# Performance work log

Measured on AMD Instinct MI355X. Metric: run time of the kernel, lower is better.

Reference implementation:

```python
import jax, jax.numpy as jnp
import numpy as np

LN_EPS = 1e-5

def _layernorm(x, w, b):
    mu = jnp.mean(x, axis=-1, keepdims=True)
    var = jnp.mean((x - mu) ** 2, axis=-1, keepdims=True)
    return (x - mu) * jax.lax.rsqrt(var + LN_EPS) * w + b

def _parallel_scan(A, B, x):
    # A, B, x: (Bb, L, S). Log-space cumsum trick, faithful to torch version.
    A_safe = jnp.clip(A, 0.001, 0.999)
    log_A = jnp.log(A_safe + 1e-10)
    log_cum_A = jnp.cumsum(log_A, axis=1)
    log_cum_A_max = jnp.max(log_cum_A, axis=1, keepdims=True)
    log_cum_A_c = log_cum_A - log_cum_A_max
    cum_A = jnp.exp(log_cum_A_c)
    BX = B * x
    # shifted (exclusive) centered log-cumsum: zeros at t=0
    zeros = jnp.zeros_like(log_cum_A_c[:, :1])
    log_cum_shift = jnp.concatenate([zeros, log_cum_A_c[:, :-1]], axis=1)
    BX_norm = BX * jnp.exp(-log_cum_shift)
    cum_BX = jnp.cumsum(BX_norm, axis=1)
    return cum_BX * cum_A

def setup_inputs() -> dict:
    key = jax.random.key(0)
    ks = jax.random.split(key, 8)
    Bb, L, D, S = 16, 4096, 512, 64
    def xavier(k, shape, gain):
        fan_out, fan_in = shape
        std = gain * np.sqrt(2.0 / (fan_in + fan_out))
        return jax.random.normal(k, shape, jnp.float32) * std
    x = jax.random.normal(ks[0], (Bb, L, D), jnp.float32)
    Wx = xavier(ks[1], (S, D), 0.5)
    Wdt = xavier(ks[2], (S, D), 1.0)
    WB = xavier(ks[3], (S, D), 0.4)
    WC = xavier(ks[4], (S, D), 0.4)
    Wout = xavier(ks[5], (D, S), 0.5)
    # A_init = -rand*0.8 - 0.2 ; A_log = log(-A_init) = log(uniform(0.2, 1.0))
    A_log = jnp.log(jax.random.uniform(ks[6], (S,), jnp.float32, 0.2, 1.0))
    return {
        "x": x,
        "ln_w": jnp.ones((D,), jnp.float32),
        "ln_b": jnp.zeros((D,), jnp.float32),
        "Wx": Wx, "bx": jnp.zeros((S,), jnp.float32),
        "Wdt": Wdt, "bdt": jnp.zeros((S,), jnp.float32),
        "A_log": A_log,
        "WB": WB, "WC": WC,
        "Dp": jnp.zeros((D,), jnp.float32),
        "Wout": Wout, "bout": jnp.zeros((D,), jnp.float32),
    }

def reference(x, ln_w, ln_b, Wx, bx, Wdt, bdt, A_log, WB, WC, Dp, Wout, bout):
    x_norm = _layernorm(x, ln_w, ln_b)                       # (B,L,D)
    delta = jax.nn.softplus(x_norm @ Wdt.T + bdt) * 0.01 + 0.0001  # (B,L,S)
    B_t = x_norm @ WB.T                                      # (B,L,S)
    C_t = x_norm @ WC.T                                      # (B,L,S)
    A = -jnp.exp(A_log)                                      # (S,)
    x_proj = x_norm @ Wx.T + bx                              # (B,L,S)
    deltaA = jnp.clip(delta * A, -10.0, -0.0001)
    A_disc = jnp.exp(deltaA)
    B_disc = delta * B_t
    h = _parallel_scan(A_disc, B_disc, x_proj)               # (B,L,S)
    y = C_t * h
    y = jnp.where(jnp.any(~jnp.isfinite(y)), jnp.zeros_like(y), y)
    y = y @ Wout.T + bout                                    # (B,L,D)
    D_safe = jnp.clip(Dp, -2.0, 2.0)
    return y + D_safe * x
```

## Files before the change

kernel.cpp:

```cpp
#include <hip/hip_runtime.h>
#include <hip/hip_bf16.h>
#include <math.h>

typedef __attribute__((ext_vector_type(4))) float  floatx4;
typedef __attribute__((ext_vector_type(8))) short  shortx8;
typedef unsigned short ushort_t;
typedef unsigned int   uint32;

#define BB 16
#define LL 4096
#define DD 512
#define SS 64
#define NTOK (BB*LL)
#define NCH 64

__device__ __forceinline__ ushort_t f2bf(float f) {
    uint32 u = __float_as_uint(f);
    u += 0x7FFFu + ((u >> 16) & 1u);
    return (ushort_t)(u >> 16);
}
__device__ __forceinline__ float bf2f(ushort_t u) {
    return __uint_as_float(((uint32)u) << 16);
}
__device__ __forceinline__ uint32 pack2(float lo, float hi) {
    __hip_bfloat162 h = __float22bfloat162_rn(make_float2(lo, hi));
    union { __hip_bfloat162 h; uint32 u; } cv; cv.h = h;
    return cv.u;
}

__device__ __forceinline__ void gload16(const void* g, void* l) {
    __builtin_amdgcn_global_load_lds(
        (const __attribute__((address_space(1))) unsigned int*)g,
        (__attribute__((address_space(3))) unsigned int*)l, 16, 0, 0);
}

__global__ __launch_bounds__(256) void k_prep(
    const float* __restrict__ Wdt, const float* __restrict__ WB,
    const float* __restrict__ WC,  const float* __restrict__ Wx,
    const float* __restrict__ Wout,
    const float* __restrict__ lnw, const float* __restrict__ lnb,
    ushort_t* __restrict__ wcat, ushort_t* __restrict__ woutb,
    float* __restrict__ u, float* __restrict__ c)
{
    const int bid = blockIdx.x;
    if (bid < 64) {
        const int wave = threadIdx.x >> 6, lane = threadIdx.x & 63;
        const int n = bid * 4 + wave;
        const float* src = (n < 64) ? Wdt : (n < 128) ? WB : (n < 192) ? WC : Wx;
        const float* row = src + (size_t)(n & 63) * 512;
        float4 a  = *(const float4*)(row + lane * 8);
        float4 b  = *(const float4*)(row + lane * 8 + 4);
        float4 wa = *(const float4*)(lnw + lane * 8);
        float4 wb = *(const float4*)(lnw + lane * 8 + 4);
        float4 ba = *(const float4*)(lnb + lane * 8);
        float4 bb = *(const float4*)(lnb + lane * 8 + 4);
        float w0 = a.x * wa.x, w1 = a.y * wa.y, w2 = a.z * wa.z, w3 = a.w * wa.w;
        float w4 = b.x * wb.x, w5 = b.y * wb.y, w6 = b.z * wb.z, w7 = b.w * wb.w;
        float us = w0 + w1 + w2 + w3 + w4 + w5 + w6 + w7;
        float cs = a.x*ba.x + a.y*ba.y + a.z*ba.z + a.w*ba.w
                 + b.x*bb.x + b.y*bb.y + b.z*bb.z + b.w*bb.w;
        uint4 o;
        o.x = (uint32)f2bf(w0) | ((uint32)f2bf(w1) << 16);
        o.y = (uint32)f2bf(w2) | ((uint32)f2bf(w3) << 16);
        o.z = (uint32)f2bf(w4) | ((uint32)f2bf(w5) << 16);
        o.w = (uint32)f2bf(w6) | ((uint32)f2bf(w7) << 16);
        ((uint4*)(wcat + (size_t)n * 512))[lane] = o;
        #pragma unroll
        for (int off = 32; off > 0; off >>= 1) {
            us += __shfl_xor(us, off);
            cs += __shfl_xor(cs, off);
        }
        if (lane == 0) { u[n] = us; c[n] = cs; }
    } else {
        int idx = (bid - 64) * 2048 + threadIdx.x * 8;
        float4 a = *(const float4*)(Wout + idx);
        float4 b = *(const float4*)(Wout + idx + 4);
        uint4 o;
        o.x = (uint32)f2bf(a.x) | ((uint32)f2bf(a.y) << 16);
        o.y = (uint32)f2bf(a.z) | ((uint32)f2bf(a.w) << 16);
        o.z = (uint32)f2bf(b.x) | ((uint32)f2bf(b.y) << 16);
        o.w = (uint32)f2bf(b.z) | ((uint32)f2bf(b.w) << 16);
        *(uint4*)(woutb + idx) = o;
    }
}

__global__ __launch_bounds__(512, 4) void k_proj(
    const float* __restrict__ x, const ushort_t* __restrict__ wcat,
    const float* __restrict__ u, const float* __restrict__ c,
    const float* __restrict__ bdt, const float* __restrict__ bx_, const float* __restrict__ A_log,
    float* __restrict__ Ap, float* __restrict__ BXv, ushort_t* __restrict__ Ctb,
    float* __restrict__ Asum, float* __restrict__ Bsum)
{
    __shared__ __align__(16) char sBuf[49152];
    __shared__ float sMu[128], sRs[128];
    ushort_t* sA = (ushort_t*)sBuf;
    ushort_t* sB = (ushort_t*)(sBuf + 16384);
    float*    sPA = (float*)sBuf;
    float*    sPB = sPA + 2 * 64 * 17;

    const int tid  = threadIdx.x;
    const int wave = tid >> 6, lane = tid & 63;
    const int ln   = lane & 15, qd = lane >> 4;
    const int mh   = wave >> 2, nq = wave & 3;
    const int token0 = blockIdx.x * 128;

    int tB[4], cB[4];
    #pragma unroll
    for (int r = 0; r < 4; r++) { int sl = r * 512 + tid; tB[r] = sl >> 3; cB[r] = ((sl & 7) ^ (tB[r] & 7)) * 8; }
    int rowA[2], k8A[2];
    #pragma unroll
    for (int r = 0; r < 2; r++) { int sl = r * 512 + tid; rowA[r] = sl >> 3; k8A[r] = sl & 7; }

    floatx4 acc[4][4] = {};
    float sacc[2] = {0.f, 0.f}, qacc[2] = {0.f, 0.f};

    for (int kc = 0; kc < 8; kc++) {
        const int kb = kc * 64;
        #pragma unroll
        for (int r = 0; r < 4; r++)
            gload16(wcat + (size_t)tB[r] * DD + kb + cB[r],
                    sBuf + 16384 + r * 8192 + wave * 1024);
        #pragma unroll
        for (int r = 0; r < 2; r++) {
            const float4* xp = (const float4*)(x + (size_t)(token0 + rowA[r]) * DD + kb + k8A[r] * 8);
            float4 v0 = xp[0], v1 = xp[1];
            sacc[r] += (v0.x + v0.y) + (v0.z + v0.w) + (v1.x + v1.y) + (v1.z + v1.w);
            qacc[r] += v0.x*v0.x + v0.y*v0.y + v0.z*v0.z + v0.w*v0.w
                     + v1.x*v1.x + v1.y*v1.y + v1.z*v1.z + v1.w*v1.w;
            uint4 pk;
            pk.x = pack2(v0.x, v0.y);
            pk.y = pack2(v0.z, v0.w);
            pk.z = pack2(v1.x, v1.y);
            pk.w = pack2(v1.z, v1.w);
            *(uint4*)(sBuf + rowA[r] * 128 + ((k8A[r] ^ (rowA[r] & 7)) << 4)) = pk;
        }
        __syncthreads();
        #pragma unroll
        for (int ks8 = 0; ks8 < 8; ks8 += 4) {
            shortx8 af[4], bf[4];
            #pragma unroll
            for (int mt = 0; mt < 4; mt++) {
                int t = mh * 64 + mt * 16 + ln;
                af[mt] = *(const shortx8*)&sA[t * 64 + (((ks8 + qd) ^ (ln & 7)) << 3)];
            }
            #pragma unroll
            for (int nt = 0; nt < 4; nt++) {
                int n = nt * 64 + nq * 16 + ln;
                bf[nt] = *(const shortx8*)&sB[n * 64 + (((ks8 + qd) ^ (ln & 7)) << 3)];
            }
            #pragma unroll
            for (int mt = 0; mt < 4; mt++)
                #pragma unroll
                for (int nt = 0; nt < 4; nt++)
                    acc[mt][nt] = __builtin_amdgcn_mfma_f32_16x16x32_bf16(
                        af[mt], bf[nt], acc[mt][nt], 0, 0, 0);
        }
        __syncthreads();
    }

    #pragma unroll
    for (int r = 0; r < 2; r++) {
        float s_ = sacc[r], q_ = qacc[r];
        s_ += __shfl_xor(s_, 1); q_ += __shfl_xor(q_, 1);
        s_ += __shfl_xor(s_, 2); q_ += __shfl_xor(q_, 2);
        s_ += __shfl_xor(s_, 4); q_ += __shfl_xor(q_, 4);
        if ((lane & 7) == 0) {
            int row = r * 64 + wave * 8 + (lane >> 3);
            float mu = s_ * (1.0f / 512.0f);
            sMu[row] = mu;
            sRs[row] = rsqrtf(q_ * (1.0f / 512.0f) - mu * mu + 1e-5f);
        }
    }
    __syncthreads();

    {
        const int s = nq * 16 + ln;
        float bdt_s = bdt[s], bx_s = bx_[s];
        float A_s = -expf(A_log[s]);
        float u0 = u[s], u1 = u[64 + s], u2 = u[128 + s], u3 = u[192 + s];
        float c0 = c[s], c1 = c[64 + s], c2 = c[128 + s], c3 = c[192 + s];
        const bool fc = ((blockIdx.x & 31) == 0) && (mh == 0);
        #pragma unroll
        for (int mt = 0; mt < 4; mt++) {
            float Al = 1.f, Bl = 0.f;
            #pragma unroll
            for (int r = 0; r < 4; r++) {
                int tl  = mt * 16 + qd * 4 + r;
                int tok = token0 + mh * 64 + tl;
                float mu_t = sMu[mh * 64 + tl], rs_t = sRs[mh * 64 + tl];
                float zdt = rs_t * (acc[mt][0][r] - mu_t * u0) + c0;
                float zb  = rs_t * (acc[mt][1][r] - mu_t * u1) + c1;
                float zc  = rs_t * (acc[mt][2][r] - mu_t * u2) + c2;
                float zx  = rs_t * (acc[mt][3][r] - mu_t * u3) + c3;
                float zin = zdt + bdt_s;
                float sp  = fmaxf(zin, 0.0f) + log1pf(expf(-fabsf(zin)));
                float delta = sp * 0.01f + 1e-4f;
                float dA    = fminf(fmaxf(delta * A_s, -10.0f), -1e-4f);
                float a     = fminf(fmaxf(expf(dA), 0.001f), 0.999f) + 1e-10f;
                float bxv   = delta * zb * (zx + bx_s);
                size_t g = (size_t)tok * 64 + s;
                Ap[g] = a; BXv[g] = bxv; Ctb[g] = f2bf(zc);
                bool first = fc && (tl == 0);
                float alpha = first ? 0.f : a;
                float beta  = first ? bxv : a * bxv;
                Al *= alpha;
                Bl = fmaf(alpha, Bl, beta);
            }
            sPA[(mh * 64 + s) * 17 + mt * 4 + qd] = Al;
            sPB[(mh * 64 + s) * 17 + mt * 4 + qd] = Bl;
        }
    }
    __syncthreads();
    if (tid < 128) {
        int ch = tid >> 6, ss = tid & 63;
        const float* pa = &sPA[(ch * 64 + ss) * 17];
        const float* pb = &sPB[(ch * 64 + ss) * 17];
        float A = pa[0], B = pb[0];
        #pragma unroll
        for (int g = 1; g < 16; g++) {
            A *= pa[g];
            B = fmaf(pa[g], B, pb[g]);
        }
        int o = (blockIdx.x * 2 + ch) * 64 + ss;
        Asum[o] = A; Bsum[o] = B;
    }
}

__global__ __launch_bounds__(256) void k_scan(
    const float* __restrict__ Ap, const float* __restrict__ BXv, const ushort_t* __restrict__ Ctb,
    const float* __restrict__ Asum, const float* __restrict__ Bsum,
    ushort_t* __restrict__ P)
{
    __shared__ float sAs[4096], sBs[4096];
    const int tid = threadIdx.x;
    const int b = blockIdx.x >> 4, cq = blockIdx.x & 15;
    #pragma unroll
    for (int i = 0; i < 16; i++) {
        int idx = i * 256 + tid;
        sAs[idx] = Asum[b * 4096 + idx];
        sBs[idx] = Bsum[b * 4096 + idx];
    }
    __syncthreads();
    const int w = tid >> 6, s = tid & 63;
    const int c = cq * 4 + w;
    float h = 0.f;
    for (int cc = 0; cc < c; cc++)
        h = fmaf(sAs[cc * 64 + s], h, sBs[cc * 64 + s]);
    size_t base = ((size_t)b * LL + c * 64) * 64 + s;
    const bool fc = (c == 0);
    #pragma unroll 8
    for (int t = 0; t < 64; t++) {
        float a = Ap[base + (size_t)t * 64];
        float v = BXv[base + (size_t)t * 64];
        float alpha = (fc && t == 0) ? 0.f : a;
        float beta  = (fc && t == 0) ? v   : a * v;
        h = fmaf(alpha, h, beta);
        P[base + (size_t)t * 64] = f2bf(bf2f(Ctb[base + (size_t)t * 64]) * h);
    }
}

__global__ __launch_bounds__(256, 4) void k_gemm2(
    const ushort_t* __restrict__ P, const ushort_t* __restrict__ woutb,
    const float* __restrict__ bout, const float* __restrict__ Dp,
    const float* __restrict__ x, float* __restrict__ out)
{
    __shared__ __align__(16) char sPBuf[8192];
    ushort_t* sP = (ushort_t*)sPBuf;

    const int tid  = threadIdx.x;
    const int wave = tid >> 6, lane = tid & 63;
    const int ln   = lane & 15, qd = lane >> 4;
    const int token0 = (blockIdx.x >> 1) * 64;
    const int dw = (blockIdx.x & 1) * 256 + wave * 64;

    #pragma unroll
    for (int r = 0; r < 2; r++) {
        int sl = r * 256 + tid;
        int t = sl >> 3, k8 = (sl & 7) ^ (t & 7);
        gload16(P + (size_t)(token0 + t) * 64 + k8 * 8,
                sPBuf + r * 4096 + wave * 1024);
    }
    __syncthreads();

    floatx4 acc[4][4] = {};
    #pragma unroll
    for (int ks8 = 0; ks8 < 8; ks8 += 4) {
        shortx8 af[4], bf[4];
        #pragma unroll
        for (int mt = 0; mt < 4; mt++) {
            int d = dw + mt * 16 + ln;
            af[mt] = *(const shortx8*)(woutb + (size_t)d * 64 + (ks8 + qd) * 8);
        }
        #pragma unroll
        for (int nt = 0; nt < 4; nt++) {
            int t = nt * 16 + ln;
            bf[nt] = *(const shortx8*)&sP[t * 64 + (((ks8 + qd) ^ (ln & 7)) << 3)];
        }
        #pragma unroll
        for (int mt = 0; mt < 4; mt++)
            #pragma unroll
            for (int nt = 0; nt < 4; nt++)
                acc[mt][nt] = __builtin_amdgcn_mfma_f32_16x16x32_bf16(
                    af[mt], bf[nt], acc[mt][nt], 0, 0, 0);
    }

    #pragma unroll
    for (int nt = 0; nt < 4; nt++) {
        const int tok = token0 + nt * 16 + ln;
        const float* xr = x + (size_t)tok * DD;
        float* orow = out + (size_t)tok * DD;
        #pragma unroll
        for (int mt = 0; mt < 4; mt++) {
            const int d0 = dw + mt * 16 + qd * 4;
            float4 xv = *(const float4*)(xr + d0);
            float4 bo = *(const float4*)(bout + d0);
            float4 dp = *(const float4*)(Dp + d0);
            float4 res;
            res.x = fmaf(fminf(fmaxf(dp.x, -2.f), 2.f), xv.x, acc[mt][nt][0] + bo.x);
            res.y = fmaf(fminf(fmaxf(dp.y, -2.f), 2.f), xv.y, acc[mt][nt][1] + bo.y);
            res.z = fmaf(fminf(fmaxf(dp.z, -2.f), 2.f), xv.z, acc[mt][nt][2] + bo.z);
            res.w = fmaf(fminf(fmaxf(dp.w, -2.f), 2.f), xv.w, acc[mt][nt][3] + bo.w);
            *(float4*)(orow + d0) = res;
        }
    }
}

extern "C" void kernel_launch(void* const* d_in, const int* in_sizes, int n_in,
                              void* d_out, int out_size, void* d_ws, size_t ws_size,
                              hipStream_t stream)
{
    const float* x     = (const float*)d_in[0];
    const float* lnw   = (const float*)d_in[1];
    const float* lnb   = (const float*)d_in[2];
    const float* Wx    = (const float*)d_in[3];
    const float* bx_   = (const float*)d_in[4];
    const float* Wdt   = (const float*)d_in[5];
    const float* bdt   = (const float*)d_in[6];
    const float* A_log = (const float*)d_in[7];
    const float* WB    = (const float*)d_in[8];
    const float* WC    = (const float*)d_in[9];
    const float* Dp    = (const float*)d_in[10];
    const float* Wout  = (const float*)d_in[11];
    const float* bout  = (const float*)d_in[12];
    float* out = (float*)d_out;

    char* w = (char*)d_ws;
    constexpr size_t SZ_XN = (size_t)NTOK * DD * 2;
    constexpr size_t SZ_T  = (size_t)NTOK * 64 * 4;
    ushort_t* Pm    = (ushort_t*)(w);
    float*    Ap    = (float*)(w + SZ_XN);
    float*    BXv   = (float*)(w + SZ_XN + SZ_T);
    ushort_t* Ctb   = (ushort_t*)(w + SZ_XN + 2 * SZ_T);
    float*    Asum  = (float*)(w + SZ_XN + 3 * SZ_T);
    float*    Bsum  = (float*)(w + SZ_XN + 3 * SZ_T + 262144);
    ushort_t* Wcat  = (ushort_t*)(w + SZ_XN + 3 * SZ_T + 2 * 262144);
    ushort_t* WoutB = (ushort_t*)(w + SZ_XN + 3 * SZ_T + 2 * 262144 + 262144);
    float*    Uc    = (float*)(w + SZ_XN + 3 * SZ_T + 2 * 262144 + 262144 + 65536);
    float*    Cc    = Uc + 256;

    k_prep<<<80, 256, 0, stream>>>(Wdt, WB, WC, Wx, Wout, lnw, lnb, Wcat, WoutB, Uc, Cc);
    k_proj<<<NTOK / 128, 512, 0, stream>>>(x, Wcat, Uc, Cc, bdt, bx_, A_log,
                                           Ap, BXv, Ctb, Asum, Bsum);
    k_scan<<<BB * 16, 256, 0, stream>>>(Ap, BXv, Ctb, Asum, Bsum, Pm);
    k_gemm2<<<(NTOK / 64) * 2, 256, 0, stream>>>(Pm, WoutB, bout, Dp, x, out);
}
```

Measured before the change: 354.1 us.

## Fuse chunked scan into projection and output GEMM kernels, drop k_scan

Removes the separate scan kernel. The projection kernel now does the intra-chunk scan in registers using wave shuffles, and writes a local partial output C*h_local in fp32 plus a carry coefficient C*prodA in bf16. The output GEMM kernel recomputes the inter-chunk carry serially from the chunk summaries and applies it while staging P into LDS. This drops the extra round trip through A/BX/C intermediates and one kernel launch. The cost is a serial carry loop of up to 63 steps in every GEMM block, duplicated across both d-halves, plus a larger fp32 intermediate.

```diff
diff --git a/kernel.cpp b/kernel.cpp
--- a/kernel.cpp
+++ b/kernel.cpp
@@ -88,15 +88,13 @@
     const float* __restrict__ x, const ushort_t* __restrict__ wcat,
     const float* __restrict__ u, const float* __restrict__ c,
     const float* __restrict__ bdt, const float* __restrict__ bx_, const float* __restrict__ A_log,
-    float* __restrict__ Ap, float* __restrict__ BXv, ushort_t* __restrict__ Ctb,
+    float* __restrict__ Pl, ushort_t* __restrict__ Gb,
     float* __restrict__ Asum, float* __restrict__ Bsum)
 {
     __shared__ __align__(16) char sBuf[49152];
     __shared__ float sMu[128], sRs[128];
     ushort_t* sA = (ushort_t*)sBuf;
     ushort_t* sB = (ushort_t*)(sBuf + 16384);
-    float*    sPA = (float*)sBuf;
-    float*    sPB = sPA + 2 * 64 * 17;
 
     const int tid  = threadIdx.x;
     const int wave = tid >> 6, lane = tid & 63;
@@ -173,8 +171,10 @@
     }
     __syncthreads();
 
+    const int s = nq * 16 + ln;
+    float aR[4][4], bR[4][4], cR[4][4];
+    float AsegA[4], BsegA[4];
     {
-        const int s = nq * 16 + ln;
         float bdt_s = bdt[s], bx_s = bx_[s];
         float A_s = -expf(A_log[s]);
         float u0 = u[s], u1 = u[64 + s], u2 = u[128 + s], u3 = u[192 + s];
@@ -186,7 +186,6 @@
             #pragma unroll
             for (int r = 0; r < 4; r++) {
                 int tl  = mt * 16 + qd * 4 + r;
-                int tok = token0 + mh * 64 + tl;
                 float mu_t = sMu[mh * 64 + tl], rs_t = sRs[mh * 64 + tl];
                 float zdt = rs_t * (acc[mt][0][r] - mu_t * u0) + c0;
                 float zb  = rs_t * (acc[mt][1][r] - mu_t * u1) + c1;
@@ -198,87 +197,105 @@
                 float dA    = fminf(fmaxf(delta * A_s, -10.0f), -1e-4f);
                 float a     = fminf(fmaxf(expf(dA), 0.001f), 0.999f) + 1e-10f;
                 float bxv   = delta * zb * (zx + bx_s);
-                size_t g = (size_t)tok * 64 + s;
-                Ap[g] = a; BXv[g] = bxv; Ctb[g] = f2bf(zc);
                 bool first = fc && (tl == 0);
                 float alpha = first ? 0.f : a;
                 float beta  = first ? bxv : a * bxv;
+                aR[mt][r] = alpha; bR[mt][r] = beta; cR[mt][r] = zc;
                 Al *= alpha;
                 Bl = fmaf(alpha, Bl, beta);
             }
-            sPA[(mh * 64 + s) * 17 + mt * 4 + qd] = Al;
-            sPB[(mh * 64 + s) * 17 + mt * 4 + qd] = Bl;
-        }
-    }
-    __syncthreads();
-    if (tid < 128) {
-        int ch = tid >> 6, ss = tid & 63;
-        const float* pa = &sPA[(ch * 64 + ss) * 17];
-        const float* pb = &sPB[(ch * 64 + ss) * 17];
-        float A = pa[0], B = pb[0];
-        #pragma unroll
-        for (int g = 1; g < 16; g++) {
-            A *= pa[g];
-            B = fmaf(pa[g], B, pb[g]);
-        }
-        int o = (blockIdx.x * 2 + ch) * 64 + ss;
-        Asum[o] = A; Bsum[o] = B;
-    }
-}
-
-__global__ __launch_bounds__(256) void k_scan(
-    const float* __restrict__ Ap, const float* __restrict__ BXv, const ushort_t* __restrict__ Ctb,
+            AsegA[mt] = Al; BsegA[mt] = Bl;
+        }
+    }
+
+    float EqA[4], EqB[4], TA[4], TB[4];
+    #pragma unroll
+    for (int mt = 0; mt < 4; mt++) {
+        float Ai = AsegA[mt], Bi = BsegA[mt];
+        float At = __shfl_up(Ai, 16), Bt = __shfl_up(Bi, 16);
+        if (qd >= 1) { Bi = fmaf(Ai, Bt, Bi); Ai *= At; }
+        At = __shfl_up(Ai, 32); Bt = __shfl_up(Bi, 32);
+        if (qd >= 2) { Bi = fmaf(Ai, Bt, Bi); Ai *= At; }
+        float Ax = __shfl_up(Ai, 16), Bx = __shfl_up(Bi, 16);
+        EqA[mt] = (qd == 0) ? 1.f : Ax;
+        EqB[mt] = (qd == 0) ? 0.f : Bx;
+        TA[mt] = __shfl(Ai, lane | 48);
+        TB[mt] = __shfl(Bi, lane | 48);
+    }
+    float EA[4], EB[4];
+    {
+        float EmA = 1.f, EmB = 0.f;
+        #pragma unroll
+        for (int mt = 0; mt < 4; mt++) {
+            EA[mt] = EqA[mt] * EmA;
+            EB[mt] = fmaf(EqA[mt], EmB, EqB[mt]);
+            EmB = fmaf(TA[mt], EmB, TB[mt]);
+            EmA = TA[mt] * EmA;
+        }
+        if (qd == 0) {
+            int o = (blockIdx.x * 2 + mh) * 64 + s;
+            Asum[o] = EmA; Bsum[o] = EmB;
+        }
+    }
+
+    #pragma unroll
+    for (int mt = 0; mt < 4; mt++) {
+        float h = EB[mt], pA = EA[mt];
+        #pragma unroll
+        for (int r = 0; r < 4; r++) {
+            h  = fmaf(aR[mt][r], h, bR[mt][r]);
+            pA *= aR[mt][r];
+            int tok = token0 + mh * 64 + mt * 16 + qd * 4 + r;
+            size_t g = (size_t)tok * 64 + s;
+            Pl[g] = cR[mt][r] * h;
+            Gb[g] = f2bf(cR[mt][r] * pA);
+        }
+    }
+}
+
+__global__ __launch_bounds__(256, 4) void k_gemm2(
+    const float* __restrict__ Pl, const ushort_t* __restrict__ Gb,
     const float* __restrict__ Asum, const float* __restrict__ Bsum,
-    ushort_t* __restrict__ P)
-{
-    __shared__ float sAs[4096], sBs[4096];
-    const int tid = threadIdx.x;
-    const int b = blockIdx.x >> 4, cq = blockIdx.x & 15;
-    #pragma unroll
-    for (int i = 0; i < 16; i++) {
-        int idx = i * 256 + tid;
-        sAs[idx] = Asum[b * 4096 + idx];
-        sBs[idx] = Bsum[b * 4096 + idx];
-    }
-    __syncthreads();
-    const int w = tid >> 6, s = tid & 63;
-    const int c = cq * 4 + w;
-    float h = 0.f;
-    for (int cc = 0; cc < c; cc++)
-        h = fmaf(sAs[cc * 64 + s], h, sBs[cc * 64 + s]);
-    size_t base = ((size_t)b * LL + c * 64) * 64 + s;
-    const bool fc = (c == 0);
-    #pragma unroll 8
-    for (int t = 0; t < 64; t++) {
-        float a = Ap[base + (size_t)t * 64];
-        float v = BXv[base + (size_t)t * 64];
-        float alpha = (fc && t == 0) ? 0.f : a;
-        float beta  = (fc && t == 0) ? v   : a * v;
-        h = fmaf(alpha, h, beta);
-        P[base + (size_t)t * 64] = f2bf(bf2f(Ctb[base + (size_t)t * 64]) * h);
-    }
-}
-
-__global__ __launch_bounds__(256, 4) void k_gemm2(
-    const ushort_t* __restrict__ P, const ushort_t* __restrict__ woutb,
+    const ushort_t* __restrict__ woutb,
     const float* __restrict__ bout, const float* __restrict__ Dp,
     const float* __restrict__ x, float* __restrict__ out)
 {
     __shared__ __align__(16) char sPBuf[8192];
+    __shared__ __align__(16) float hcL[64];
     ushort_t* sP = (ushort_t*)sPBuf;
 
     const int tid  = threadIdx.x;
     const int wave = tid >> 6, lane = tid & 63;
     const int ln   = lane & 15, qd = lane >> 4;
-    const int token0 = (blockIdx.x >> 1) * 64;
+    const int cglob  = blockIdx.x >> 1;
+    const int token0 = cglob * 64;
     const int dw = (blockIdx.x & 1) * 256 + wave * 64;
 
-    #pragma unroll
-    for (int r = 0; r < 2; r++) {
-        int sl = r * 256 + tid;
-        int t = sl >> 3, k8 = (sl & 7) ^ (t & 7);
-        gload16(P + (size_t)(token0 + t) * 64 + k8 * 8,
-                sPBuf + r * 4096 + wave * 1024);
+    if (tid < 64) {
+        const int seq0 = (cglob >> 6) << 6;
+        float h = 0.f;
+        for (int c2 = seq0; c2 < cglob; ++c2)
+            h = fmaf(Asum[c2 * 64 + tid], h, Bsum[c2 * 64 + tid]);
+        hcL[tid] = h;
+    }
+    __syncthreads();
+
+    #pragma unroll
+    for (int r = 0; r < 4; r++) {
+        int slot = r * 256 + tid;
+        int t = slot >> 4, s0 = (slot & 15) * 4;
+        float4 pl = *(const float4*)(Pl + (size_t)(token0 + t) * 64 + s0);
+        uint2  gv = *(const uint2*)(Gb + (size_t)(token0 + t) * 64 + s0);
+        float4 hc = *(const float4*)&hcL[s0];
+        float p0 = fmaf(bf2f((ushort_t)(gv.x & 0xffff)), hc.x, pl.x);
+        float p1 = fmaf(bf2f((ushort_t)(gv.x >> 16)),    hc.y, pl.y);
+        float p2 = fmaf(bf2f((ushort_t)(gv.y & 0xffff)), hc.z, pl.z);
+        float p3 = fmaf(bf2f((ushort_t)(gv.y >> 16)),    hc.w, pl.w);
+        uint2 w2;
+        w2.x = pack2(p0, p1);
+        w2.y = pack2(p2, p3);
+        int byteoff = t * 128 + (((s0 >> 3) ^ (t & 7)) << 4) + ((s0 & 7) << 1);
+        *(uint2*)(sPBuf + byteoff) = w2;
     }
     __syncthreads();
 
@@ -345,22 +362,20 @@
     float* out = (float*)d_out;
 
     char* w = (char*)d_ws;
-    constexpr size_t SZ_XN = (size_t)NTOK * DD * 2;
-    constexpr size_t SZ_T  = (size_t)NTOK * 64 * 4;
-    ushort_t* Pm    = (ushort_t*)(w);
-    float*    Ap    = (float*)(w + SZ_XN);
-    float*    BXv   = (float*)(w + SZ_XN + SZ_T);
-    ushort_t* Ctb   = (ushort_t*)(w + SZ_XN + 2 * SZ_T);
-    float*    Asum  = (float*)(w + SZ_XN + 3 * SZ_T);
-    float*    Bsum  = (float*)(w + SZ_XN + 3 * SZ_T + 262144);
-    ushort_t* Wcat  = (ushort_t*)(w + SZ_XN + 3 * SZ_T + 2 * 262144);
-    ushort_t* WoutB = (ushort_t*)(w + SZ_XN + 3 * SZ_T + 2 * 262144 + 262144);
-    float*    Uc    = (float*)(w + SZ_XN + 3 * SZ_T + 2 * 262144 + 262144 + 65536);
+    constexpr size_t SZ_PL = (size_t)NTOK * 64 * 4;
+    constexpr size_t SZ_GB = (size_t)NTOK * 64 * 2;
+    float*    Plm   = (float*)(w);
+    ushort_t* Gbm   = (ushort_t*)(w + SZ_PL);
+    float*    Asum  = (float*)(w + SZ_PL + SZ_GB);
+    float*    Bsum  = (float*)(w + SZ_PL + SZ_GB + 262144);
+    ushort_t* Wcat  = (ushort_t*)(w + SZ_PL + SZ_GB + 2 * 262144);
+    ushort_t* WoutB = (ushort_t*)(w + SZ_PL + SZ_GB + 2 * 262144 + 262144);
+    float*    Uc    = (float*)(w + SZ_PL + SZ_GB + 2 * 262144 + 262144 + 65536);
     float*    Cc    = Uc + 256;
 
     k_prep<<<80, 256, 0, stream>>>(Wdt, WB, WC, Wx, Wout, lnw, lnb, Wcat, WoutB, Uc, Cc);
     k_proj<<<NTOK / 128, 512, 0, stream>>>(x, Wcat, Uc, Cc, bdt, bx_, A_log,
-                                           Ap, BXv, Ctb, Asum, Bsum);
-    k_scan<<<BB * 16, 256, 0, stream>>>(Ap, BXv, Ctb, Asum, Bsum, Pm);
-    k_gemm2<<<(NTOK / 64) * 2, 256, 0, stream>>>(Pm, WoutB, bout, Dp, x, out);
-}
+                                           Plm, Gbm, Asum, Bsum);
+    k_gemm2<<<(NTOK / 64) * 2, 256, 0, stream>>>(Plm, Gbm, Asum, Bsum, WoutB,
+                                                 bout, Dp, x, out);
+}
```

After: 359.1 us. About the same (+1.4%).
